# Kernel optimization log

Measured on AMD Instinct MI355X. Metric: run time of the kernel, lower is better.

The kernel has to match this reference:

```python
import jax, jax.numpy as jnp
import numpy as np

N, E, D, L, RBF = 20000, 320000, 128, 3, 64
CUTOFF = 5.0
LN_EPS = 1e-5


def setup_inputs() -> dict:
    key = jax.random.key(0)
    ks = jax.random.split(key, 20)
    s = 0.05
    inp = {
        'z': jax.random.normal(ks[0], (N, 64), jnp.float32),
        'pos': jax.random.normal(ks[1], (N, 3), jnp.float32),
        'edge_index': jax.random.randint(ks[2], (2, E), 0, N),
        'in_w': jax.random.normal(ks[3], (64, D), jnp.float32) * s,
        'in_b': jnp.zeros((D,), jnp.float32),
        'filt_w': jax.random.normal(ks[4], (RBF, 3 * D), jnp.float32) * s,
        'filt_b': jnp.zeros((3 * D,), jnp.float32),
        'inter_w1': jax.random.normal(ks[5], (L, D, D), jnp.float32) * s,
        'inter_b1': jnp.zeros((L, D), jnp.float32),
        'inter_w2': jax.random.normal(ks[6], (L, D, 3 * D), jnp.float32) * s,
        'inter_b2': jnp.zeros((L, 3 * D), jnp.float32),
        'mix_mu_w': jax.random.normal(ks[7], (L, D, 2 * D), jnp.float32) * s,
        'mix_w1': jax.random.normal(ks[8], (L, 2 * D, D), jnp.float32) * s,
        'mix_b1': jnp.zeros((L, D), jnp.float32),
        'mix_w2': jax.random.normal(ks[9], (L, D, 3 * D), jnp.float32) * s,
        'mix_b2': jnp.zeros((L, 3 * D), jnp.float32),
        'mu_proj_w': jnp.zeros((D,), jnp.float32),  # nn.init.constant_(0.0) in source
        'ln_g': jnp.ones((D,), jnp.float32),
        'ln_b': jnp.zeros((D,), jnp.float32),
    }
    return inp


def painn_forward(z, pos, in_w, in_b, filt_w, filt_b, inter_w1, inter_b1,
                  inter_w2, inter_b2, mix_mu_w, mix_w1, mix_b1, mix_w2, mix_b2,
                  mu_proj_w, ln_g, ln_b, edge_index):
    idx_i, idx_j = edge_index[0], edge_index[1]
    # edge geometry
    r_ij = pos[idx_j] - pos[idx_i]                               # [E,3]
    d_ij = jnp.maximum(jnp.linalg.norm(r_ij, axis=1, keepdims=True), 1e-8)  # [E,1]
    dir_ij = r_ij / d_ij                                          # [E,3]
    # gaussian smearing
    offset = jnp.linspace(0.0, CUTOFF, RBF).astype(jnp.float32)
    coeff = -0.5 / (offset[1] - offset[0]) ** 2
    phi = jnp.exp(coeff * (d_ij - offset) ** 2)                   # [E,RBF]
    # cosine cutoff
    xc = jnp.clip(d_ij / CUTOFF, 0.0, 1.0)
    fcut = 0.5 * (jnp.cos(jnp.pi * xc) + 1.0) * (xc < 1.0)        # [E,1]
    filters = (phi @ filt_w + filt_b) * fcut                      # [E,3D]
    filters = jnp.clip(jnp.nan_to_num(filters), -5.0, 5.0)
    Wij = filters[:, None, :]                                     # [E,1,3D]

    q = jax.nn.silu(z @ in_w + in_b)[:, None, :]                  # [N,1,D]
    mu = jnp.zeros((N, 3, D), q.dtype)                            # [N,3,D]

    for l in range(L):
        # interaction (edge gather -> gate -> scatter-add)
        x = jax.nn.silu(q @ inter_w1[l] + inter_b1[l]) @ inter_w2[l] + inter_b2[l]  # [N,1,3D]
        xj = x[idx_j] * Wij                                       # [E,1,3D]
        dq, dmuR, dmumu = jnp.split(xj, 3, axis=-1)               # each [E,1,D]
        muj = mu[idx_j]                                           # [E,3,D]
        q = q + jax.ops.segment_sum(dq, idx_i, num_segments=N)
        dmu = dmuR * dir_ij[:, :, None] + dmumu * muj             # [E,3,D]
        mu = mu + jax.ops.segment_sum(dmu, idx_i, num_segments=N)
        # intra-atomic mixing
        mu_mix = mu @ mix_mu_w[l]                                  # [N,3,2D]
        mu_V, mu_W = jnp.split(mu_mix, 2, axis=-1)                 # [N,3,D]
        mu_Vn = jnp.sqrt(jnp.sum(mu_V ** 2, axis=-2, keepdims=True) + 1e-8)  # [N,1,D]
        ctx = jnp.concatenate([q, mu_Vn], axis=-1)                 # [N,1,2D]
        xm = jax.nn.silu(ctx @ mix_w1[l] + mix_b1[l]) @ mix_w2[l] + mix_b2[l]  # [N,1,3D]
        dq_i, dmu_i, dqmu_i = jnp.split(xm, 3, axis=-1)
        q = q + dq_i + dqmu_i * jnp.sum(mu_V * mu_W, axis=1, keepdims=True)
        mu = mu + dmu_i * mu_W

    node_attr = jnp.clip(jnp.nan_to_num(q[:, 0, :]), -5.0, 5.0)   # [N,D]
    mean = jnp.mean(node_attr, axis=-1, keepdims=True)
    var = jnp.var(node_attr, axis=-1, keepdims=True)
    node_attr = (node_attr - mean) * jax.lax.rsqrt(var + LN_EPS) * ln_g + ln_b
    node_attr = jnp.nan_to_num(jnp.tanh(node_attr))

    mu = jnp.nan_to_num(mu)
    mu_node = jax.ops.segment_sum(mu[idx_j], idx_i, num_segments=N)  # [N,3,D]
    mu_node = jnp.clip(jnp.nan_to_num(mu_node), -5.0, 5.0)
    pos_attr = jnp.clip(jnp.nan_to_num(mu_node @ mu_proj_w), -5.0, 5.0)  # [N,3]
    return node_attr, pos_attr


def reference(z, pos, edge_index, in_w, in_b, filt_w, filt_b, inter_w1, inter_b1,
              inter_w2, inter_b2, mix_mu_w, mix_w1, mix_b1, mix_w2, mix_b2,
              mu_proj_w, ln_g, ln_b):
    return painn_forward(z, pos, in_w, in_b, filt_w, filt_b, inter_w1, inter_b1,
                         inter_w2, inter_b2, mix_mu_w, mix_w1, mix_b1, mix_w2,
                         mix_b2, mu_proj_w, ln_g, ln_b, edge_index)
```

## Files before the change

### kernel.cpp

```cpp
#include <hip/hip_runtime.h>
#include <math.h>

#ifndef M_PI
#define M_PI 3.14159265358979323846
#endif

static constexpr int N_NODES = 20000;
static constexpr int N_EDGES = 320000;
static constexpr int NLAYER  = 3;
static constexpr int NB_SCAN = (N_NODES + 255) / 256;
static constexpr int TAB_T   = 1024;

typedef _Float16 f16;
typedef __attribute__((ext_vector_type(2))) _Float16 f16x2;
typedef __attribute__((ext_vector_type(8))) _Float16 f16x8;
typedef __attribute__((ext_vector_type(4))) float f32x4;

__device__ __forceinline__ void storev(float* p, float v) { *p = v; }
__device__ __forceinline__ void storev(f16* p, float v)   { *p = (f16)v; }

__global__ void k_hist(const int* __restrict__ idx_i, int* __restrict__ cnt) {
  int e = blockIdx.x * 256 + threadIdx.x;
  if (e < N_EDGES) atomicAdd(&cnt[idx_i[e]], 1);
}

__global__ void k_scan_blk(const int* __restrict__ cnt, int* __restrict__ incl,
                           int* __restrict__ bsum) {
  __shared__ int buf[256];
  int t = threadIdx.x;
  int i = blockIdx.x * 256 + t;
  int v = (i < N_NODES) ? cnt[i] : 0;
  buf[t] = v;
  __syncthreads();
  #pragma unroll
  for (int off = 1; off < 256; off <<= 1) {
    int x = (t >= off) ? buf[t - off] : 0;
    __syncthreads();
    buf[t] += x;
    __syncthreads();
  }
  if (i < N_NODES) incl[i] = buf[t];
  if (t == 255) bsum[blockIdx.x] = buf[255];
}

__global__ void k_scan_top(int* __restrict__ bsum) {
  __shared__ int buf[128];
  int t = threadIdx.x;
  int v = (t < NB_SCAN) ? bsum[t] : 0;
  buf[t] = v;
  __syncthreads();
  #pragma unroll
  for (int off = 1; off < 128; off <<= 1) {
    int x = (t >= off) ? buf[t - off] : 0;
    __syncthreads();
    buf[t] += x;
    __syncthreads();
  }
  if (t <= NB_SCAN) bsum[t] = buf[t] - v;
}

__global__ void k_scan_add(const int* __restrict__ cnt, const int* __restrict__ incl,
                           const int* __restrict__ bsum, int* __restrict__ rs,
                           int* __restrict__ cur) {
  int i = blockIdx.x * 256 + threadIdx.x;
  if (i < N_NODES) {
    int v = bsum[blockIdx.x] + incl[i] - cnt[i];
    rs[i] = v;
    cur[i] = v;
  }
  if (i == 0) rs[N_NODES] = bsum[NB_SCAN];
}

__global__ void k_fill(const int* __restrict__ idx_i, int* __restrict__ cur, int* __restrict__ eidx) {
  int e = blockIdx.x * 256 + threadIdx.x;
  if (e < N_EDGES) {
    int p = atomicAdd(&cur[idx_i[e]], 1);
    eidx[p] = e;
  }
}

__global__ void k_edge_geom(const float* __restrict__ pos, const int* __restrict__ idx_all,
                            const int* __restrict__ eidx, float4* __restrict__ geo,
                            int* __restrict__ jperm) {
  int p = blockIdx.x * 256 + threadIdx.x;
  if (p >= N_EDGES) return;
  int e = eidx[p];
  int i = idx_all[e];
  int j = idx_all[N_EDGES + e];
  float rx = pos[j*3+0] - pos[i*3+0];
  float ry = pos[j*3+1] - pos[i*3+1];
  float rz = pos[j*3+2] - pos[i*3+2];
  float d = sqrtf(rx*rx + ry*ry + rz*rz);
  d = fmaxf(d, 1e-8f);
  float inv = 1.0f / d;
  geo[p] = make_float4(d, rx*inv, ry*inv, rz*inv);
  jperm[p] = j;
}

struct WJob { const float* src; f16* dst; int kshift; int ld; int col0; int nk; };
struct WJobs { WJob j[17]; };

__global__ void k_wt_all(WJobs jb) {
  WJob w = jb.j[blockIdx.y];
  int t = blockIdx.x * 256 + threadIdx.x;
  if (t >= w.nk) return;
  int K = 1 << w.kshift;
  int n = t >> w.kshift;
  int k = t & (K - 1);
  w.dst[t] = (f16)w.src[(size_t)k * w.ld + w.col0 + n];
}

__global__ __launch_bounds__(128) void k_tab(const f16* __restrict__ wt_f ,
                                             const float* __restrict__ bias,
                                             f16* __restrict__ tab) {
  __shared__ float ph[64];
  const int t = blockIdx.x;
  const float dist = 5.0f * (float)t / (float)(TAB_T - 1);
  const int tid = threadIdx.x;
  const float delta = 5.0f / 63.0f;
  const float coeff = -0.5f / (delta * delta);
  if (tid < 64) {
    float u = dist - delta * (float)tid;
    ph[tid] = expf(coeff * u * u);
  }
  __syncthreads();
  float xc = dist * 0.2f;
  float fc = (xc < 1.0f) ? 0.5f * (cosf((float)M_PI * xc) + 1.0f) : 0.0f;
  #pragma unroll
  for (int s = 0; s < 3; ++s) {
    int n = tid + s * 128;
    const f16* wr = wt_f + (size_t)n * 64;
    float acc = 0.f;
    #pragma unroll
    for (int k = 0; k < 64; ++k) acc += ph[k] * (float)wr[k];
    float v = (acc + bias[n]) * fc;
    v = fminf(fmaxf(v, -5.0f), 5.0f);
    tab[(size_t)t * 384 + n] = (f16)v;
  }
}

template<int EPI, typename AT, typename CT>
__global__ __launch_bounds__(256) void k_mgemm(
    const AT* __restrict__ A, const f16* __restrict__ Wt,
    const float* __restrict__ bias, CT* __restrict__ C,
    int M, int K, int ldc) {
  __shared__ f16 As[128 * 32];
  __shared__ f16 Bs[128 * 32];
  const int bm = blockIdx.x * 128;
  const int bn = blockIdx.y * 128;
  const int tid = threadIdx.x;
  const int wave = tid >> 6, lane = tid & 63;
  const int wm = (wave & 1) * 64, wn = (wave >> 1) * 64;
  const int lr = lane & 15;
  const int lk = lane >> 4;
  const int srow = tid >> 1;
  const int sc0 = (tid & 1) * 2;
  const int sw = (srow >> 1) & 3;
  f32x4 acc[4][4] = {};
  for (int k0 = 0; k0 < K; k0 += 32) {
    {
      int gm = bm + srow;
      f16x8 c0, c1;
      if (gm < M) {
        if constexpr (sizeof(AT) == 2) {
          const f16* ap = (const f16*)A + (size_t)gm * K + k0 + sc0 * 8;
          c0 = *(const f16x8*)ap;
          c1 = *(const f16x8*)(ap + 8);
        } else {
          const float* ap = (const float*)A + (size_t)gm * K + k0 + sc0 * 8;
          float4 v0 = ((const float4*)ap)[0];
          float4 v1 = ((const float4*)ap)[1];
          float4 v2 = ((const float4*)ap)[2];
          float4 v3 = ((const float4*)ap)[3];
          c0[0]=(f16)v0.x; c0[1]=(f16)v0.y; c0[2]=(f16)v0.z; c0[3]=(f16)v0.w;
          c0[4]=(f16)v1.x; c0[5]=(f16)v1.y; c0[6]=(f16)v1.z; c0[7]=(f16)v1.w;
          c1[0]=(f16)v2.x; c1[1]=(f16)v2.y; c1[2]=(f16)v2.z; c1[3]=(f16)v2.w;
          c1[4]=(f16)v3.x; c1[5]=(f16)v3.y; c1[6]=(f16)v3.z; c1[7]=(f16)v3.w;
        }
      } else {
        #pragma unroll
        for (int u = 0; u < 8; ++u) { c0[u] = (f16)0.f; c1[u] = (f16)0.f; }
      }
      *(f16x8*)&As[srow * 32 + ((sc0 ^ sw) << 3)]       = c0;
      *(f16x8*)&As[srow * 32 + (((sc0 + 1) ^ sw) << 3)] = c1;
    }
    {
      const f16* bp = Wt + (size_t)(bn + srow) * K + k0 + sc0 * 8;
      f16x8 b0 = *(const f16x8*)bp;
      f16x8 b1 = *(const f16x8*)(bp + 8);
      *(f16x8*)&Bs[srow * 32 + ((sc0 ^ sw) << 3)]       = b0;
      *(f16x8*)&Bs[srow * 32 + (((sc0 + 1) ^ sw) << 3)] = b1;
    }
    __syncthreads();
    f16x8 af[4], bf[4];
    #pragma unroll
    for (int mt = 0; mt < 4; ++mt) {
      int r = wm + mt * 16 + lr;
      af[mt] = *(const f16x8*)&As[r * 32 + ((lk ^ ((r >> 1) & 3)) << 3)];
    }
    #pragma unroll
    for (int nt = 0; nt < 4; ++nt) {
      int r = wn + nt * 16 + lr;
      bf[nt] = *(const f16x8*)&Bs[r * 32 + ((lk ^ ((r >> 1) & 3)) << 3)];
    }
    #pragma unroll
    for (int mt = 0; mt < 4; ++mt)
      #pragma unroll
      for (int nt = 0; nt < 4; ++nt)
        acc[mt][nt] = __builtin_amdgcn_mfma_f32_16x16x32_f16(af[mt], bf[nt], acc[mt][nt], 0, 0, 0);
    __syncthreads();
  }
  #pragma unroll
  for (int mt = 0; mt < 4; ++mt) {
    int gm0 = bm + wm + mt * 16 + lk * 4;
    #pragma unroll
    for (int nt = 0; nt < 4; ++nt) {
      int gn = bn + wn + nt * 16 + lr;
      float bv = bias ? bias[gn] : 0.0f;
      #pragma unroll
      for (int rr = 0; rr < 4; ++rr) {
        int gm = gm0 + rr;
        if (gm >= M) continue;
        float v = acc[mt][nt][rr] + bv;
        if (EPI == 1) v = v / (1.0f + expf(-v));
        storev(&C[(size_t)gm * ldc + gn], v);
      }
    }
  }
}

__global__ __launch_bounds__(256) void k_fused_i(
    const float* __restrict__ q, const f16* __restrict__ W1, const float* __restrict__ b1,
    const f16* __restrict__ W2, const float* __restrict__ b2,
    f16* __restrict__ xout, int M) {
  __shared__ f16 As[64 * 32];
  __shared__ f16 Hs[64 * 132];
  const int tid = threadIdx.x;
  const int wave = tid >> 6, lane = tid & 63;
  const int wm = (wave & 1) * 32, wn = (wave >> 1) * 64;
  const int lr = lane & 15, lk = lane >> 4;
  const int srow = tid >> 2, c8 = tid & 3;
  const int sw = (srow >> 1) & 3;
  const int bm = blockIdx.x * 64;
  f32x4 acc[2][4] = {};
  for (int k0 = 0; k0 < 128; k0 += 32) {
    {
      int gm = bm + srow;
      f16x8 c0;
      if (gm < M) {
        const float* ap = q + (size_t)gm * 128 + k0 + c8 * 8;
        float4 v0 = ((const float4*)ap)[0];
        float4 v1 = ((const float4*)ap)[1];
        c0[0]=(f16)v0.x; c0[1]=(f16)v0.y; c0[2]=(f16)v0.z; c0[3]=(f16)v0.w;
        c0[4]=(f16)v1.x; c0[5]=(f16)v1.y; c0[6]=(f16)v1.z; c0[7]=(f16)v1.w;
      } else {
        #pragma unroll
        for (int u = 0; u < 8; ++u) c0[u] = (f16)0.f;
      }
      *(f16x8*)&As[srow * 32 + ((c8 ^ sw) << 3)] = c0;
    }
    __syncthreads();
    f16x8 af[2], bf[4];
    #pragma unroll
    for (int mt = 0; mt < 2; ++mt) {
      int r = wm + mt * 16 + lr;
      af[mt] = *(const f16x8*)&As[r * 32 + ((lk ^ ((r >> 1) & 3)) << 3)];
    }
    #pragma unroll
    for (int nt = 0; nt < 4; ++nt)
      bf[nt] = *(const f16x8*)&W1[(size_t)(wn + nt * 16 + lr) * 128 + k0 + lk * 8];
    #pragma unroll
    for (int mt = 0; mt < 2; ++mt)
      #pragma unroll
      for (int nt = 0; nt < 4; ++nt)
        acc[mt][nt] = __builtin_amdgcn_mfma_f32_16x16x32_f16(af[mt], bf[nt], acc[mt][nt], 0, 0, 0);
    __syncthreads();
  }
  #pragma unroll
  for (int mt = 0; mt < 2; ++mt)
    #pragma unroll
    for (int nt = 0; nt < 4; ++nt) {
      int col = wn + nt * 16 + lr;
      float bv = b1[col];
      #pragma unroll
      for (int rr = 0; rr < 4; ++rr) {
        int row = wm + mt * 16 + lk * 4 + rr;
        float v = acc[mt][nt][rr] + bv;
        v = v / (1.0f + expf(-v));
        Hs[row * 132 + col] = (f16)v;
      }
    }
  __syncthreads();
  #pragma unroll
  for (int cc = 0; cc < 3; ++cc) {
    f32x4 a2[2][4] = {};
    for (int k0 = 0; k0 < 128; k0 += 32) {
      f16x8 af2[2], bf2[4];
      #pragma unroll
      for (int mt = 0; mt < 2; ++mt)
        af2[mt] = *(const f16x8*)&Hs[(wm + mt * 16 + lr) * 132 + k0 + lk * 8];
      #pragma unroll
      for (int nt = 0; nt < 4; ++nt)
        bf2[nt] = *(const f16x8*)&W2[(size_t)(cc * 128 + wn + nt * 16 + lr) * 128 + k0 + lk * 8];
      #pragma unroll
      for (int mt = 0; mt < 2; ++mt)
        #pragma unroll
        for (int nt = 0; nt < 4; ++nt)
          a2[mt][nt] = __builtin_amdgcn_mfma_f32_16x16x32_f16(af2[mt], bf2[nt], a2[mt][nt], 0, 0, 0);
    }
    #pragma unroll
    for (int mt = 0; mt < 2; ++mt)
      #pragma unroll
      for (int nt = 0; nt < 4; ++nt) {
        int gn = cc * 128 + wn + nt * 16 + lr;
        float bv = b2[gn];
        #pragma unroll
        for (int rr = 0; rr < 4; ++rr) {
          int gm = bm + wm + mt * 16 + lk * 4 + rr;
          if (gm >= M) continue;
          xout[(size_t)gm * 384 + gn] = (f16)(a2[mt][nt][rr] + bv);
        }
      }
  }
}

__global__ __launch_bounds__(256) void k_fused_mx(
    float* __restrict__ q, f16* __restrict__ mu,
    const f16* __restrict__ Wmu,
    const f16* __restrict__ W1, const float* __restrict__ b1,
    const f16* __restrict__ W2, const float* __restrict__ b2) {
  __shared__ __align__(16) char pool[50688 + 24576];
  f16* MM  = (f16*)pool;
  f16* As4 = (f16*)(pool + 50688);
  f16* VN  = (f16*)(pool + 50688);
  f16* HS  = (f16*)(pool + 50688 + 8192);

  const int tid = threadIdx.x;
  const int wave = tid >> 6, lane = tid & 63;
  const int lr = lane & 15, lk = lane >> 4;
  const int n0 = blockIdx.x * 32;
  const int r0 = n0 * 3;

  #pragma unroll
  for (int rep = 0; rep < 6; ++rep) {
    int idx = rep * 256 + tid;
    int row = idx >> 4;
    int g   = idx & 15;
    int kb = g >> 2, c8 = g & 3;
    f16x8 v = *(const f16x8*)(mu + (size_t)(r0 + row) * 128 + g * 8);
    *(f16x8*)&As4[((kb * 96 + row) << 5) + (((c8 ^ ((row >> 1) & 3))) << 3)] = v;
  }
  __syncthreads();

  const int wmA = (wave & 1) * 48;
  const int wnA0 = (wave >> 1) * 64;
  #pragma unroll
  for (int half = 0; half < 2; ++half) {
    f32x4 accA[3][4] = {};
    #pragma unroll
    for (int kk = 0; kk < 4; ++kk) {
      f16x8 af[3], bf[4];
      #pragma unroll
      for (int mt = 0; mt < 3; ++mt) {
        int r = wmA + mt * 16 + lr;
        af[mt] = *(const f16x8*)&As4[((kk * 96 + r) << 5) + ((lk ^ ((r >> 1) & 3)) << 3)];
      }
      #pragma unroll
      for (int nt = 0; nt < 4; ++nt)
        bf[nt] = *(const f16x8*)&Wmu[(size_t)(half * 128 + wnA0 + nt * 16 + lr) * 128 + kk * 32 + lk * 8];
      #pragma unroll
      for (int mt = 0; mt < 3; ++mt)
        #pragma unroll
        for (int nt = 0; nt < 4; ++nt)
          accA[mt][nt] = __builtin_amdgcn_mfma_f32_16x16x32_f16(af[mt], bf[nt], accA[mt][nt], 0, 0, 0);
    }
    #pragma unroll
    for (int mt = 0; mt < 3; ++mt)
      #pragma unroll
      for (int nt = 0; nt < 4; ++nt) {
        int col = half * 128 + wnA0 + nt * 16 + lr;
        #pragma unroll
        for (int rr = 0; rr < 4; ++rr) {
          int row = wmA + mt * 16 + lk * 4 + rr;
          MM[row * 264 + col] = (f16)accA[mt][nt][rr];
        }
      }
  }
  __syncthreads();

  #pragma unroll
  for (int rep = 0; rep < 16; ++rep) {
    int idx = rep * 256 + tid;
    int nn = idx >> 7, c = idx & 127;
    float V0 = (float)MM[(nn * 3 + 0) * 264 + c];
    float V1 = (float)MM[(nn * 3 + 1) * 264 + c];
    float V2 = (float)MM[(nn * 3 + 2) * 264 + c];
    float vnv = sqrtf(V0 * V0 + V1 * V1 + V2 * V2 + 1e-8f);
    int kb = c >> 5, c8 = (c >> 3) & 3, ce = c & 7;
    VN[((kb * 32 + nn) << 5) + ((c8 ^ ((nn >> 1) & 3)) << 3) + ce] = (f16)vnv;
  }
  __syncthreads();

  const int wmB = (wave & 1) * 16, wnB = (wave >> 1) * 64;
  f32x4 accB[4] = {};
  #pragma unroll
  for (int kk = 0; kk < 8; ++kk) {
    f16x8 af;
    int row = wmB + lr;
    if (kk < 4) {
      const float* qp_ = q + (size_t)(n0 + row) * 128 + kk * 32 + lk * 8;
      float4 v0 = ((const float4*)qp_)[0];
      float4 v1 = ((const float4*)qp_)[1];
      af[0]=(f16)v0.x; af[1]=(f16)v0.y; af[2]=(f16)v0.z; af[3]=(f16)v0.w;
      af[4]=(f16)v1.x; af[5]=(f16)v1.y; af[6]=(f16)v1.z; af[7]=(f16)v1.w;
    } else {
      af = *(const f16x8*)&VN[(((kk - 4) * 32 + row) << 5) + ((lk ^ ((row >> 1) & 3)) << 3)];
    }
    f16x8 bf[4];
    #pragma unroll
    for (int nt = 0; nt < 4; ++nt)
      bf[nt] = *(const f16x8*)&W1[(size_t)(wnB + nt * 16 + lr) * 256 + kk * 32 + lk * 8];
    #pragma unroll
    for (int nt = 0; nt < 4; ++nt)
      accB[nt] = __builtin_amdgcn_mfma_f32_16x16x32_f16(af, bf[nt], accB[nt], 0, 0, 0);
  }
  #pragma unroll
  for (int nt = 0; nt < 4; ++nt) {
    int col = wnB + nt * 16 + lr;
    float bv = b1[col];
    #pragma unroll
    for (int rr = 0; rr < 4; ++rr) {
      int row = wmB + lk * 4 + rr;
      float v = accB[nt][rr] + bv;
      v = v / (1.0f + expf(-v));
      HS[row * 132 + col] = (f16)v;
    }
  }
  __syncthreads();

  f32x4 accC[3][4] = {};
  #pragma unroll
  for (int cc = 0; cc < 3; ++cc)
    #pragma unroll
    for (int kk = 0; kk < 4; ++kk) {
      f16x8 af = *(const f16x8*)&HS[(wmB + lr) * 132 + kk * 32 + lk * 8];
      f16x8 bf[4];
      #pragma unroll
      for (int nt = 0; nt < 4; ++nt)
        bf[nt] = *(const f16x8*)&W2[(size_t)(cc * 128 + wnB + nt * 16 + lr) * 128 + kk * 32 + lk * 8];
      #pragma unroll
      for (int nt = 0; nt < 4; ++nt)
        accC[cc][nt] = __builtin_amdgcn_mfma_f32_16x16x32_f16(af, bf[nt], accC[cc][nt], 0, 0, 0);
    }
  #pragma unroll
  for (int nt = 0; nt < 4; ++nt) {
    int col = wnB + nt * 16 + lr;
    float b_dq = b2[col], b_dmu = b2[128 + col], b_dqmu = b2[256 + col];
    #pragma unroll
    for (int rr = 0; rr < 4; ++rr) {
      int nn = wmB + lk * 4 + rr;
      int gm = n0 + nn;
      float dq   = accC[0][nt][rr] + b_dq;
      float dmu  = accC[1][nt][rr] + b_dmu;
      float dqmu = accC[2][nt][rr] + b_dqmu;
      float V0 = (float)MM[(nn * 3 + 0) * 264 + col], W0 = (float)MM[(nn * 3 + 0) * 264 + 128 + col];
      float V1 = (float)MM[(nn * 3 + 1) * 264 + col], W1v = (float)MM[(nn * 3 + 1) * 264 + 128 + col];
      float V2 = (float)MM[(nn * 3 + 2) * 264 + col], W2v = (float)MM[(nn * 3 + 2) * 264 + 128 + col];
      float svw = V0 * W0 + V1 * W1v + V2 * W2v;
      size_t qi = (size_t)gm * 128 + col;
      q[qi] += dq + dqmu * svw;
      f16* mr = mu + (size_t)gm * 384;
      mr[col]       = (f16)((float)mr[col]       + dmu * W0);
      mr[128 + col] = (f16)((float)mr[128 + col] + dmu * W1v);
      mr[256 + col] = (f16)((float)mr[256 + col] + dmu * W2v);
    }
  }
}

__global__ __launch_bounds__(256) void k_edge_msg(
    const int* __restrict__ rs, const int* __restrict__ jperm,
    const f16* __restrict__ x, const f16* __restrict__ tab,
    const float4* __restrict__ geo, const f16* __restrict__ mu_in,
    float* __restrict__ q, f16* __restrict__ mu_out) {
  const int wid  = threadIdx.x >> 6;
  const int lane = threadIdx.x & 63;
  const int i = blockIdx.x * 4 + wid;
  if (i >= N_NODES) return;
  const int d0 = lane * 2;
  const float scale = (float)(TAB_T - 1) / 5.0f;
  float aqx = 0.f, aqy = 0.f;
  float a0x = 0.f, a0y = 0.f, a1x = 0.f, a1y = 0.f, a2x = 0.f, a2y = 0.f;
  const int s = rs[i], e = rs[i + 1];

  auto body = [&](float dx, float dy, float dz,
                  f16x2 ta0, f16x2 ta1, f16x2 ta2, f16x2 tb0, f16x2 tb1, f16x2 tb2,
                  f16x2 xv0, f16x2 xv1, f16x2 xv2, f16x2 mv0, f16x2 mv1, f16x2 mv2,
                  float fr) {
    float fo = 1.0f - fr;
    float W0x = fo * (float)ta0[0] + fr * (float)tb0[0];
    float W0y = fo * (float)ta0[1] + fr * (float)tb0[1];
    float W1x = fo * (float)ta1[0] + fr * (float)tb1[0];
    float W1y = fo * (float)ta1[1] + fr * (float)tb1[1];
    float W2x = fo * (float)ta2[0] + fr * (float)tb2[0];
    float W2y = fo * (float)ta2[1] + fr * (float)tb2[1];
    float m1x = (float)xv1[0] * W1x, m1y = (float)xv1[1] * W1y;
    float m2x = (float)xv2[0] * W2x, m2y = (float)xv2[1] * W2y;
    aqx = fmaf((float)xv0[0], W0x, aqx);
    aqy = fmaf((float)xv0[1], W0y, aqy);
    a0x += m1x * dx + m2x * (float)mv0[0];
    a0y += m1y * dx + m2y * (float)mv0[1];
    a1x += m1x * dy + m2x * (float)mv1[0];
    a1y += m1y * dy + m2y * (float)mv1[1];
    a2x += m1x * dz + m2x * (float)mv2[0];
    a2y += m1y * dz + m2y * (float)mv2[1];
  };

  int p = s;
  for (; p + 2 <= e; p += 2) {
    int jA = jperm[p], jB = jperm[p + 1];
    float4 gA = geo[p], gB = geo[p + 1];
    float uA = fminf(gA.x, 5.0f) * scale;
    float uB = fminf(gB.x, 5.0f) * scale;
    int tA = min((int)uA, TAB_T - 2);
    int tB = min((int)uB, TAB_T - 2);
    float frA = uA - (float)tA, frB = uB - (float)tB;
    const f16* taA = tab + (size_t)tA * 384;
    const f16* taB = tab + (size_t)tB * 384;
    const f16* xjA = x + (size_t)jA * 384;
    const f16* xjB = x + (size_t)jB * 384;
    const f16* mjA = mu_in + (size_t)jA * 384;
    const f16* mjB = mu_in + (size_t)jB * 384;
    f16x2 tA0 = *(const f16x2*)(taA + d0);
    f16x2 tA1 = *(const f16x2*)(taA + 128 + d0);
    f16x2 tA2 = *(const f16x2*)(taA + 256 + d0);
    f16x2 tA3 = *(const f16x2*)(taA + 384 + d0);
    f16x2 tA4 = *(const f16x2*)(taA + 512 + d0);
    f16x2 tA5 = *(const f16x2*)(taA + 640 + d0);
    f16x2 xA0 = *(const f16x2*)(xjA + d0);
    f16x2 xA1 = *(const f16x2*)(xjA + 128 + d0);
    f16x2 xA2 = *(const f16x2*)(xjA + 256 + d0);
    f16x2 mA0 = *(const f16x2*)(mjA + d0);
    f16x2 mA1 = *(const f16x2*)(mjA + 128 + d0);
    f16x2 mA2 = *(const f16x2*)(mjA + 256 + d0);
    f16x2 tB0 = *(const f16x2*)(taB + d0);
    f16x2 tB1 = *(const f16x2*)(taB + 128 + d0);
    f16x2 tB2 = *(const f16x2*)(taB + 256 + d0);
    f16x2 tB3 = *(const f16x2*)(taB + 384 + d0);
    f16x2 tB4 = *(const f16x2*)(taB + 512 + d0);
    f16x2 tB5 = *(const f16x2*)(taB + 640 + d0);
    f16x2 xB0 = *(const f16x2*)(xjB + d0);
    f16x2 xB1 = *(const f16x2*)(xjB + 128 + d0);
    f16x2 xB2 = *(const f16x2*)(xjB + 256 + d0);
    f16x2 mB0 = *(const f16x2*)(mjB + d0);
    f16x2 mB1 = *(const f16x2*)(mjB + 128 + d0);
    f16x2 mB2 = *(const f16x2*)(mjB + 256 + d0);
    body(gA.y, gA.z, gA.w, tA0, tA1, tA2, tA3, tA4, tA5,
         xA0, xA1, xA2, mA0, mA1, mA2, frA);
    body(gB.y, gB.z, gB.w, tB0, tB1, tB2, tB3, tB4, tB5,
         xB0, xB1, xB2, mB0, mB1, mB2, frB);
  }
  for (; p < e; ++p) {
    int j = jperm[p];
    float4 g = geo[p];
    float u = fminf(g.x, 5.0f) * scale;
    int t0 = min((int)u, TAB_T - 2);
    float fr = u - (float)t0;
    const f16* ta = tab + (size_t)t0 * 384;
    const f16* xj = x + (size_t)j * 384;
    const f16* mj = mu_in + (size_t)j * 384;
    body(g.y, g.z, g.w,
         *(const f16x2*)(ta + d0), *(const f16x2*)(ta + 128 + d0), *(const f16x2*)(ta + 256 + d0),
         *(const f16x2*)(ta + 384 + d0), *(const f16x2*)(ta + 512 + d0), *(const f16x2*)(ta + 640 + d0),
         *(const f16x2*)(xj + d0), *(const f16x2*)(xj + 128 + d0), *(const f16x2*)(xj + 256 + d0),
         *(const f16x2*)(mj + d0), *(const f16x2*)(mj + 128 + d0), *(const f16x2*)(mj + 256 + d0),
         fr);
  }

  float* qp = q + (size_t)i * 128 + d0;
  float2 qv = *(float2*)qp;
  qv.x += aqx; qv.y += aqy;
  *(float2*)qp = qv;
  const f16* min_ = mu_in + (size_t)i * 384;
  f16* mout = mu_out + (size_t)i * 384;
  f16x2 o0, o1, o2;
  f16x2 i0 = *(const f16x2*)(min_ + d0);
  f16x2 i1 = *(const f16x2*)(min_ + 128 + d0);
  f16x2 i2 = *(const f16x2*)(min_ + 256 + d0);
  o0[0] = (f16)((float)i0[0] + a0x); o0[1] = (f16)((float)i0[1] + a0y);
  o1[0] = (f16)((float)i1[0] + a1x); o1[1] = (f16)((float)i1[1] + a1y);
  o2[0] = (f16)((float)i2[0] + a2x); o2[1] = (f16)((float)i2[1] + a2y);
  *(f16x2*)(mout + d0)       = o0;
  *(f16x2*)(mout + 128 + d0) = o1;
  *(f16x2*)(mout + 256 + d0) = o2;
}

__global__ __launch_bounds__(256) void k_posattr(
    const int* __restrict__ rs, const int* __restrict__ jperm,
    const f16* __restrict__ mu, const float* __restrict__ w, float* __restrict__ pos_out) {
  const int wid  = threadIdx.x >> 6;
  const int lane = threadIdx.x & 63;
  const int i = blockIdx.x * 4 + wid;
  if (i >= N_NODES) return;
  const int d0 = lane * 2;
  float a0x = 0.f, a0y = 0.f, a1x = 0.f, a1y = 0.f, a2x = 0.f, a2y = 0.f;
  const int s = rs[i], e = rs[i + 1];
  int p = s;
  for (; p + 2 <= e; p += 2) {
    int jA = jperm[p], jB = jperm[p + 1];
    const f16* mA = mu + (size_t)jA * 384;
    const f16* mB = mu + (size_t)jB * 384;
    f16x2 A0 = *(const f16x2*)(mA + d0);
    f16x2 A1 = *(const f16x2*)(mA + 128 + d0);
    f16x2 A2 = *(const f16x2*)(mA + 256 + d0);
    f16x2 B0 = *(const f16x2*)(mB + d0);
    f16x2 B1 = *(const f16x2*)(mB + 128 + d0);
    f16x2 B2 = *(const f16x2*)(mB + 256 + d0);
    a0x += (float)A0[0] + (float)B0[0]; a0y += (float)A0[1] + (float)B0[1];
    a1x += (float)A1[0] + (float)B1[0]; a1y += (float)A1[1] + (float)B1[1];
    a2x += (float)A2[0] + (float)B2[0]; a2y += (float)A2[1] + (float)B2[1];
  }
  for (; p < e; ++p) {
    int j = jperm[p];
    const f16* mj = mu + (size_t)j * 384;
    f16x2 A0 = *(const f16x2*)(mj + d0);
    f16x2 A1 = *(const f16x2*)(mj + 128 + d0);
    f16x2 A2 = *(const f16x2*)(mj + 256 + d0);
    a0x += (float)A0[0]; a0y += (float)A0[1];
    a1x += (float)A1[0]; a1y += (float)A1[1];
    a2x += (float)A2[0]; a2y += (float)A2[1];
  }
  float wx = w[d0], wy = w[d0 + 1];
  float s0 = fminf(fmaxf(a0x, -5.f), 5.f) * wx + fminf(fmaxf(a0y, -5.f), 5.f) * wy;
  float s1 = fminf(fmaxf(a1x, -5.f), 5.f) * wx + fminf(fmaxf(a1y, -5.f), 5.f) * wy;
  float s2 = fminf(fmaxf(a2x, -5.f), 5.f) * wx + fminf(fmaxf(a2y, -5.f), 5.f) * wy;
  #pragma unroll
  for (int off = 32; off > 0; off >>= 1) {
    s0 += __shfl_down(s0, off, 64);
    s1 += __shfl_down(s1, off, 64);
    s2 += __shfl_down(s2, off, 64);
  }
  if (lane == 0) {
    pos_out[(size_t)i * 3 + 0] = fminf(fmaxf(s0, -5.f), 5.f);
    pos_out[(size_t)i * 3 + 1] = fminf(fmaxf(s1, -5.f), 5.f);
    pos_out[(size_t)i * 3 + 2] = fminf(fmaxf(s2, -5.f), 5.f);
  }
}

__global__ __launch_bounds__(256) void k_ln(const float* __restrict__ q, const float* __restrict__ g,
                                            const float* __restrict__ b, float* __restrict__ out) {
  const int wid = threadIdx.x >> 6, lane = threadIdx.x & 63;
  const int n = blockIdx.x * 4 + wid;
  if (n >= N_NODES) return;
  const int d0 = lane * 2;
  float2 v = *(const float2*)(q + (size_t)n * 128 + d0);
  float v0 = fminf(fmaxf(v.x, -5.f), 5.f);
  float v1 = fminf(fmaxf(v.y, -5.f), 5.f);
  float s = v0 + v1, s2 = v0 * v0 + v1 * v1;
  #pragma unroll
  for (int off = 32; off > 0; off >>= 1) {
    s  += __shfl_down(s,  off, 64);
    s2 += __shfl_down(s2, off, 64);
  }
  s  = __shfl(s,  0, 64);
  s2 = __shfl(s2, 0, 64);
  float mean = s * (1.0f / 128.0f);
  float var  = s2 * (1.0f / 128.0f) - mean * mean;
  float r = rsqrtf(var + 1e-5f);
  out[(size_t)n * 128 + d0]     = tanhf((v0 - mean) * r * g[d0]     + b[d0]);
  out[(size_t)n * 128 + d0 + 1] = tanhf((v1 - mean) * r * g[d0 + 1] + b[d0 + 1]);
}

extern "C" void kernel_launch(void* const* d_in, const int* in_sizes, int n_in,
                              void* d_out, int out_size, void* d_ws, size_t ws_size,
                              hipStream_t stream) {
  const float* z         = (const float*)d_in[0];
  const float* pos       = (const float*)d_in[1];
  const int*   edge_idx  = (const int*)d_in[2];
  const float* in_w      = (const float*)d_in[3];
  const float* in_b      = (const float*)d_in[4];
  const float* filt_w    = (const float*)d_in[5];
  const float* filt_b    = (const float*)d_in[6];
  const float* inter_w1  = (const float*)d_in[7];
  const float* inter_b1  = (const float*)d_in[8];
  const float* inter_w2  = (const float*)d_in[9];
  const float* inter_b2  = (const float*)d_in[10];
  const float* mix_mu_w  = (const float*)d_in[11];
  const float* mix_w1    = (const float*)d_in[12];
  const float* mix_b1    = (const float*)d_in[13];
  const float* mix_w2    = (const float*)d_in[14];
  const float* mix_b2    = (const float*)d_in[15];
  const float* mu_proj_w = (const float*)d_in[16];
  const float* ln_g      = (const float*)d_in[17];
  const float* ln_b      = (const float*)d_in[18];

  char* base = (char*)d_ws;
  size_t off = 0;
  auto alloc = [&](size_t bytes) -> char* {
    char* p = base + off;
    off += (bytes + 255) & ~(size_t)255;
    return p;
  };
  float*  q     = (float*)alloc((size_t)N_NODES * 128 * 4);
  f16*    x16   = (f16*)alloc((size_t)N_NODES * 384 * 2);
  f16*    mu_a  = (f16*)alloc((size_t)N_NODES * 384 * 2);
  f16*    mu_b  = (f16*)alloc((size_t)N_NODES * 384 * 2);
  float4* geo   = (float4*)alloc((size_t)N_EDGES * 16);
  int*    cnt   = (int*)alloc((size_t)N_NODES * 4);
  int*    incl  = (int*)alloc((size_t)N_NODES * 4);
  int*    bsum  = (int*)alloc(128 * 4);
  int*    rs    = (int*)alloc((size_t)(N_NODES + 1) * 4);
  int*    cur   = (int*)alloc((size_t)N_NODES * 4);
  int*    eidx  = (int*)alloc((size_t)N_EDGES * 4);
  int*    jperm = (int*)alloc((size_t)N_EDGES * 4);
  f16*    tab   = (f16*)alloc((size_t)TAB_T * 384 * 2);
  f16* wt_in = (f16*)alloc((size_t)128 * 64 * 2);
  f16* wt_f  = (f16*)alloc((size_t)384 * 64 * 2);
  f16* wt_i1 = (f16*)alloc((size_t)3 * 128 * 128 * 2);
  f16* wt_i2 = (f16*)alloc((size_t)3 * 384 * 128 * 2);
  f16* wt_mu = (f16*)alloc((size_t)3 * 256 * 128 * 2);
  f16* wt_x1 = (f16*)alloc((size_t)3 * 128 * 256 * 2);
  f16* wt_x2 = (f16*)alloc((size_t)3 * 384 * 128 * 2);
  if (off > ws_size) return;

  float* out_node = (float*)d_out;
  float* out_pos  = (float*)d_out + (size_t)N_NODES * 128;

  {
    WJobs jb;
    int ji = 0;
    jb.j[ji++] = {in_w,   wt_in, 6, 128, 0, 128 * 64};
    jb.j[ji++] = {filt_w, wt_f,  6, 384, 0, 384 * 64};
    for (int l = 0; l < 3; ++l)
      jb.j[ji++] = {inter_w1 + (size_t)l*128*128, wt_i1 + (size_t)l*128*128, 7, 128, 0, 128*128};
    for (int l = 0; l < 3; ++l)
      jb.j[ji++] = {inter_w2 + (size_t)l*128*384, wt_i2 + (size_t)l*384*128, 7, 384, 0, 384*128};
    for (int l = 0; l < 3; ++l)
      jb.j[ji++] = {mix_mu_w + (size_t)l*128*256, wt_mu + (size_t)l*256*128, 7, 256, 0, 256*128};
    for (int l = 0; l < 3; ++l)
      jb.j[ji++] = {mix_w1 + (size_t)l*256*128, wt_x1 + (size_t)l*128*256, 8, 128, 0, 128*256};
    for (int l = 0; l < 3; ++l)
      jb.j[ji++] = {mix_w2 + (size_t)l*128*384, wt_x2 + (size_t)l*384*128, 7, 384, 0, 384*128};
    dim3 g(192, 17);
    k_wt_all<<<g, 256, 0, stream>>>(jb);
  }

  k_tab<<<TAB_T, 128, 0, stream>>>(wt_f, filt_b, tab);

  hipMemsetAsync(cnt, 0, (size_t)N_NODES * 4, stream);
  k_hist<<<N_EDGES / 256, 256, 0, stream>>>(edge_idx, cnt);
  k_scan_blk<<<NB_SCAN, 256, 0, stream>>>(cnt, incl, bsum);
  k_scan_top<<<1, 128, 0, stream>>>(bsum);
  k_scan_add<<<NB_SCAN, 256, 0, stream>>>(cnt, incl, bsum, rs, cur);
  k_fill<<<N_EDGES / 256, 256, 0, stream>>>(edge_idx, cur, eidx);

  k_edge_geom<<<N_EDGES / 256, 256, 0, stream>>>(pos, edge_idx, eidx, geo, jperm);

  dim3 ge((N_NODES + 127) / 128, 1);
  k_mgemm<1, float, float><<<ge, 256, 0, stream>>>(z, wt_in, in_b, q, N_NODES, 64, 128);
  hipMemsetAsync(mu_a, 0, (size_t)N_NODES * 384 * 2, stream);

  f16* mu_cur = mu_a;
  f16* mu_nxt = mu_b;
  const int gn4 = (N_NODES + 3) / 4;
  const int gf  = (N_NODES + 63) / 64;
  const int gmx = N_NODES / 32;
  for (int l = 0; l < NLAYER; ++l) {
    k_fused_i<<<gf, 256, 0, stream>>>(q, wt_i1 + (size_t)l*128*128, inter_b1 + (size_t)l*128,
                                      wt_i2 + (size_t)l*384*128, inter_b2 + (size_t)l*384,
                                      x16, N_NODES);
    k_edge_msg<<<gn4, 256, 0, stream>>>(rs, jperm, x16, tab, geo, mu_cur, q, mu_nxt);
    { f16* t = mu_cur; mu_cur = mu_nxt; mu_nxt = t; }
    k_fused_mx<<<gmx, 256, 0, stream>>>(q, mu_cur, wt_mu + (size_t)l*256*128,
                                        wt_x1 + (size_t)l*128*256, mix_b1 + (size_t)l*128,
                                        wt_x2 + (size_t)l*384*128, mix_b2 + (size_t)l*384);
  }

  k_posattr<<<gn4, 256, 0, stream>>>(rs, jperm, mu_cur, mu_proj_w, out_pos);
  k_ln<<<gn4, 256, 0, stream>>>(q, ln_g, ln_b, out_node);
}
```

Measured before the change: 613.5 us.

## Merge setup kernels, skip zero mu work in first layer, fuse output kernels

```diff
diff --git a/kernel.cpp b/kernel.cpp
--- a/kernel.cpp
+++ b/kernel.cpp
@@ -71,22 +71,14 @@
   if (i == 0) rs[N_NODES] = bsum[NB_SCAN];
 }
 
-__global__ void k_fill(const int* __restrict__ idx_i, int* __restrict__ cur, int* __restrict__ eidx) {
+__global__ void k_fill_geom(const int* __restrict__ idx_all, const float* __restrict__ pos,
+                            int* __restrict__ cur, float4* __restrict__ geo,
+                            int* __restrict__ jperm) {
   int e = blockIdx.x * 256 + threadIdx.x;
-  if (e < N_EDGES) {
-    int p = atomicAdd(&cur[idx_i[e]], 1);
-    eidx[p] = e;
-  }
-}
-
-__global__ void k_edge_geom(const float* __restrict__ pos, const int* __restrict__ idx_all,
-                            const int* __restrict__ eidx, float4* __restrict__ geo,
-                            int* __restrict__ jperm) {
-  int p = blockIdx.x * 256 + threadIdx.x;
-  if (p >= N_EDGES) return;
-  int e = eidx[p];
+  if (e >= N_EDGES) return;
   int i = idx_all[e];
   int j = idx_all[N_EDGES + e];
+  int p = atomicAdd(&cur[i], 1);
   float rx = pos[j*3+0] - pos[i*3+0];
   float ry = pos[j*3+1] - pos[i*3+1];
   float rz = pos[j*3+2] - pos[i*3+2];
@@ -98,25 +90,26 @@
 }
 
 struct WJob { const float* src; f16* dst; int kshift; int ld; int col0; int nk; };
-struct WJobs { WJob j[17]; };
-
-__global__ void k_wt_all(WJobs jb) {
-  WJob w = jb.j[blockIdx.y];
-  int t = blockIdx.x * 256 + threadIdx.x;
-  if (t >= w.nk) return;
-  int K = 1 << w.kshift;
-  int n = t >> w.kshift;
-  int k = t & (K - 1);
-  w.dst[t] = (f16)w.src[(size_t)k * w.ld + w.col0 + n];
-}
-
-__global__ __launch_bounds__(128) void k_tab(const f16* __restrict__ wt_f ,
-                                             const float* __restrict__ bias,
-                                             f16* __restrict__ tab) {
+struct WJobs { WJob j[16]; };
+
+__global__ __launch_bounds__(256) void k_prep(WJobs jb, const float* __restrict__ filt_w,
+                                              const float* __restrict__ filt_b,
+                                              f16* __restrict__ tab) {
+  if (blockIdx.y < 16) {
+    WJob w = jb.j[blockIdx.y];
+    int t = blockIdx.x * 256 + threadIdx.x;
+    if (t >= w.nk) return;
+    int K = 1 << w.kshift;
+    int n = t >> w.kshift;
+    int k = t & (K - 1);
+    w.dst[t] = (f16)w.src[(size_t)k * w.ld + w.col0 + n];
+    return;
+  }
+  if (blockIdx.x >= 128) return;
+  const int t = (blockIdx.y - 16) * 128 + blockIdx.x;
   __shared__ float ph[64];
-  const int t = blockIdx.x;
+  const int tid = threadIdx.x;
   const float dist = 5.0f * (float)t / (float)(TAB_T - 1);
-  const int tid = threadIdx.x;
   const float delta = 5.0f / 63.0f;
   const float coeff = -0.5f / (delta * delta);
   if (tid < 64) {
@@ -126,14 +119,11 @@
   __syncthreads();
   float xc = dist * 0.2f;
   float fc = (xc < 1.0f) ? 0.5f * (cosf((float)M_PI * xc) + 1.0f) : 0.0f;
-  #pragma unroll
-  for (int s = 0; s < 3; ++s) {
-    int n = tid + s * 128;
-    const f16* wr = wt_f + (size_t)n * 64;
+  for (int n = tid; n < 384; n += 256) {
     float acc = 0.f;
     #pragma unroll
-    for (int k = 0; k < 64; ++k) acc += ph[k] * (float)wr[k];
-    float v = (acc + bias[n]) * fc;
+    for (int k = 0; k < 64; ++k) acc += ph[k] * filt_w[k * 384 + n];
+    float v = (acc + filt_b[n]) * fc;
     v = fminf(fmaxf(v, -5.0f), 5.0f);
     tab[(size_t)t * 384 + n] = (f16)v;
   }
@@ -477,6 +467,7 @@
   }
 }
 
+template<bool HASMU>
 __global__ __launch_bounds__(256) void k_edge_msg(
     const int* __restrict__ rs, const int* __restrict__ jperm,
     const f16* __restrict__ x, const f16* __restrict__ tab,
@@ -492,116 +483,104 @@
   float a0x = 0.f, a0y = 0.f, a1x = 0.f, a1y = 0.f, a2x = 0.f, a2y = 0.f;
   const int s = rs[i], e = rs[i + 1];
 
-  auto body = [&](float dx, float dy, float dz,
-                  f16x2 ta0, f16x2 ta1, f16x2 ta2, f16x2 tb0, f16x2 tb1, f16x2 tb2,
-                  f16x2 xv0, f16x2 xv1, f16x2 xv2, f16x2 mv0, f16x2 mv1, f16x2 mv2,
-                  float fr) {
-    float fo = 1.0f - fr;
+  for (int p = s; p < e; ++p) {
+    int j = jperm[p];
+    float4 g = geo[p];
+    float u = fminf(g.x, 5.0f) * scale;
+    int t0 = min((int)u, TAB_T - 2);
+    float fr = u - (float)t0, fo = 1.0f - fr;
+    const f16* ta = tab + (size_t)t0 * 384;
+    const f16* xj = x + (size_t)j * 384;
+    f16x2 ta0 = *(const f16x2*)(ta + d0);
+    f16x2 ta1 = *(const f16x2*)(ta + 128 + d0);
+    f16x2 tb0 = *(const f16x2*)(ta + 384 + d0);
+    f16x2 tb1 = *(const f16x2*)(ta + 512 + d0);
+    f16x2 xv0 = *(const f16x2*)(xj + d0);
+    f16x2 xv1 = *(const f16x2*)(xj + 128 + d0);
     float W0x = fo * (float)ta0[0] + fr * (float)tb0[0];
     float W0y = fo * (float)ta0[1] + fr * (float)tb0[1];
     float W1x = fo * (float)ta1[0] + fr * (float)tb1[0];
     float W1y = fo * (float)ta1[1] + fr * (float)tb1[1];
-    float W2x = fo * (float)ta2[0] + fr * (float)tb2[0];
-    float W2y = fo * (float)ta2[1] + fr * (float)tb2[1];
     float m1x = (float)xv1[0] * W1x, m1y = (float)xv1[1] * W1y;
-    float m2x = (float)xv2[0] * W2x, m2y = (float)xv2[1] * W2y;
     aqx = fmaf((float)xv0[0], W0x, aqx);
     aqy = fmaf((float)xv0[1], W0y, aqy);
-    a0x += m1x * dx + m2x * (float)mv0[0];
-    a0y += m1y * dx + m2y * (float)mv0[1];
-    a1x += m1x * dy + m2x * (float)mv1[0];
-    a1y += m1y * dy + m2y * (float)mv1[1];
-    a2x += m1x * dz + m2x * (float)mv2[0];
-    a2y += m1y * dz + m2y * (float)mv2[1];
-  };
-
-  int p = s;
-  for (; p + 2 <= e; p += 2) {
-    int jA = jperm[p], jB = jperm[p + 1];
-    float4 gA = geo[p], gB = geo[p + 1];
-    float uA = fminf(gA.x, 5.0f) * scale;
-    float uB = fminf(gB.x, 5.0f) * scale;
-    int tA = min((int)uA, TAB_T - 2);
-    int tB = min((int)uB, TAB_T - 2);
-    float frA = uA - (float)tA, frB = uB - (float)tB;
-    const f16* taA = tab + (size_t)tA * 384;
-    const f16* taB = tab + (size_t)tB * 384;
-    const f16* xjA = x + (size_t)jA * 384;
-    const f16* xjB = x + (size_t)jB * 384;
-    const f16* mjA = mu_in + (size_t)jA * 384;
-    const f16* mjB = mu_in + (size_t)jB * 384;
-    f16x2 tA0 = *(const f16x2*)(taA + d0);
-    f16x2 tA1 = *(const f16x2*)(taA + 128 + d0);
-    f16x2 tA2 = *(const f16x2*)(taA + 256 + d0);
-    f16x2 tA3 = *(const f16x2*)(taA + 384 + d0);
-    f16x2 tA4 = *(const f16x2*)(taA + 512 + d0);
-    f16x2 tA5 = *(const f16x2*)(taA + 640 + d0);
-    f16x2 xA0 = *(const f16x2*)(xjA + d0);
-    f16x2 xA1 = *(const f16x2*)(xjA + 128 + d0);
-    f16x2 xA2 = *(const f16x2*)(xjA + 256 + d0);
-    f16x2 mA0 = *(const f16x2*)(mjA + d0);
-    f16x2 mA1 = *(const f16x2*)(mjA + 128 + d0);
-    f16x2 mA2 = *(const f16x2*)(mjA + 256 + d0);
-    f16x2 tB0 = *(const f16x2*)(taB + d0);
-    f16x2 tB1 = *(const f16x2*)(taB + 128 + d0);
-    f16x2 tB2 = *(const f16x2*)(taB + 256 + d0);
-    f16x2 tB3 = *(const f16x2*)(taB + 384 + d0);
-    f16x2 tB4 = *(const f16x2*)(taB + 512 + d0);
-    f16x2 tB5 = *(const f16x2*)(taB + 640 + d0);
-    f16x2 xB0 = *(const f16x2*)(xjB + d0);
-    f16x2 xB1 = *(const f16x2*)(xjB + 128 + d0);
-    f16x2 xB2 = *(const f16x2*)(xjB + 256 + d0);
-    f16x2 mB0 = *(const f16x2*)(mjB + d0);
-    f16x2 mB1 = *(const f16x2*)(mjB + 128 + d0);
-    f16x2 mB2 = *(const f16x2*)(mjB + 256 + d0);
-    body(gA.y, gA.z, gA.w, tA0, tA1, tA2, tA3, tA4, tA5,
-         xA0, xA1, xA2, mA0, mA1, mA2, frA);
-    body(gB.y, gB.z, gB.w, tB0, tB1, tB2, tB3, tB4, tB5,
-         xB0, xB1, xB2, mB0, mB1, mB2, frB);
-  }
-  for (; p < e; ++p) {
-    int j = jperm[p];
-    float4 g = geo[p];
-    float u = fminf(g.x, 5.0f) * scale;
-    int t0 = min((int)u, TAB_T - 2);
-    float fr = u - (float)t0;
-    const f16* ta = tab + (size_t)t0 * 384;
-    const f16* xj = x + (size_t)j * 384;
-    const f16* mj = mu_in + (size_t)j * 384;
-    body(g.y, g.z, g.w,
-         *(const f16x2*)(ta + d0), *(const f16x2*)(ta + 128 + d0), *(const f16x2*)(ta + 256 + d0),
-         *(const f16x2*)(ta + 384 + d0), *(const f16x2*)(ta + 512 + d0), *(const f16x2*)(ta + 640 + d0),
-         *(const f16x2*)(xj + d0), *(const f16x2*)(xj + 128 + d0), *(const f16x2*)(xj + 256 + d0),
-         *(const f16x2*)(mj + d0), *(const f16x2*)(mj + 128 + d0), *(const f16x2*)(mj + 256 + d0),
-         fr);
+    if constexpr (HASMU) {
+      f16x2 ta2 = *(const f16x2*)(ta + 256 + d0);
+      f16x2 tb2 = *(const f16x2*)(ta + 640 + d0);
+      f16x2 xv2 = *(const f16x2*)(xj + 256 + d0);
+      const f16* mj = mu_in + (size_t)j * 384;
+      f16x2 mv0 = *(const f16x2*)(mj + d0);
+      f16x2 mv1 = *(const f16x2*)(mj + 128 + d0);
+      f16x2 mv2 = *(const f16x2*)(mj + 256 + d0);
+      float W2x = fo * (float)ta2[0] + fr * (float)tb2[0];
+      float W2y = fo * (float)ta2[1] + fr * (float)tb2[1];
+      float m2x = (float)xv2[0] * W2x, m2y = (float)xv2[1] * W2y;
+      a0x += m1x * g.y + m2x * (float)mv0[0];
+      a0y += m1y * g.y + m2y * (float)mv0[1];
+      a1x += m1x * g.z + m2x * (float)mv1[0];
+      a1y += m1y * g.z + m2y * (float)mv1[1];
+      a2x += m1x * g.w + m2x * (float)mv2[0];
+      a2y += m1y * g.w + m2y * (float)mv2[1];
+    } else {
+      a0x += m1x * g.y; a0y += m1y * g.y;
+      a1x += m1x * g.z; a1y += m1y * g.z;
+      a2x += m1x * g.w; a2y += m1y * g.w;
+    }
   }
 
   float* qp = q + (size_t)i * 128 + d0;
   float2 qv = *(float2*)qp;
   qv.x += aqx; qv.y += aqy;
   *(float2*)qp = qv;
-  const f16* min_ = mu_in + (size_t)i * 384;
   f16* mout = mu_out + (size_t)i * 384;
   f16x2 o0, o1, o2;
-  f16x2 i0 = *(const f16x2*)(min_ + d0);
-  f16x2 i1 = *(const f16x2*)(min_ + 128 + d0);
-  f16x2 i2 = *(const f16x2*)(min_ + 256 + d0);
-  o0[0] = (f16)((float)i0[0] + a0x); o0[1] = (f16)((float)i0[1] + a0y);
-  o1[0] = (f16)((float)i1[0] + a1x); o1[1] = (f16)((float)i1[1] + a1y);
-  o2[0] = (f16)((float)i2[0] + a2x); o2[1] = (f16)((float)i2[1] + a2y);
+  if constexpr (HASMU) {
+    const f16* min_ = mu_in + (size_t)i * 384;
+    f16x2 i0 = *(const f16x2*)(min_ + d0);
+    f16x2 i1 = *(const f16x2*)(min_ + 128 + d0);
+    f16x2 i2 = *(const f16x2*)(min_ + 256 + d0);
+    o0[0] = (f16)((float)i0[0] + a0x); o0[1] = (f16)((float)i0[1] + a0y);
+    o1[0] = (f16)((float)i1[0] + a1x); o1[1] = (f16)((float)i1[1] + a1y);
+    o2[0] = (f16)((float)i2[0] + a2x); o2[1] = (f16)((float)i2[1] + a2y);
+  } else {
+    o0[0] = (f16)a0x; o0[1] = (f16)a0y;
+    o1[0] = (f16)a1x; o1[1] = (f16)a1y;
+    o2[0] = (f16)a2x; o2[1] = (f16)a2y;
+  }
   *(f16x2*)(mout + d0)       = o0;
   *(f16x2*)(mout + 128 + d0) = o1;
   *(f16x2*)(mout + 256 + d0) = o2;
 }
 
-__global__ __launch_bounds__(256) void k_posattr(
+__global__ __launch_bounds__(256) void k_outputs(
     const int* __restrict__ rs, const int* __restrict__ jperm,
-    const f16* __restrict__ mu, const float* __restrict__ w, float* __restrict__ pos_out) {
+    const f16* __restrict__ mu, const float* __restrict__ w, float* __restrict__ pos_out,
+    const float* __restrict__ q, const float* __restrict__ g_, const float* __restrict__ b_,
+    float* __restrict__ out_node) {
   const int wid  = threadIdx.x >> 6;
   const int lane = threadIdx.x & 63;
   const int i = blockIdx.x * 4 + wid;
   if (i >= N_NODES) return;
   const int d0 = lane * 2;
+  if (blockIdx.y == 1) {
+    float2 v = *(const float2*)(q + (size_t)i * 128 + d0);
+    float v0 = fminf(fmaxf(v.x, -5.f), 5.f);
+    float v1 = fminf(fmaxf(v.y, -5.f), 5.f);
+    float s = v0 + v1, s2 = v0 * v0 + v1 * v1;
+    #pragma unroll
+    for (int off = 32; off > 0; off >>= 1) {
+      s  += __shfl_down(s,  off, 64);
+      s2 += __shfl_down(s2, off, 64);
+    }
+    s  = __shfl(s,  0, 64);
+    s2 = __shfl(s2, 0, 64);
+    float mean = s * (1.0f / 128.0f);
+    float var  = s2 * (1.0f / 128.0f) - mean * mean;
+    float r = rsqrtf(var + 1e-5f);
+    out_node[(size_t)i * 128 + d0]     = tanhf((v0 - mean) * r * g_[d0]     + b_[d0]);
+    out_node[(size_t)i * 128 + d0 + 1] = tanhf((v1 - mean) * r * g_[d0 + 1] + b_[d0 + 1]);
+    return;
+  }
   float a0x = 0.f, a0y = 0.f, a1x = 0.f, a1y = 0.f, a2x = 0.f, a2y = 0.f;
   const int s = rs[i], e = rs[i + 1];
   int p = s;
@@ -644,30 +623,6 @@
     pos_out[(size_t)i * 3 + 1] = fminf(fmaxf(s1, -5.f), 5.f);
     pos_out[(size_t)i * 3 + 2] = fminf(fmaxf(s2, -5.f), 5.f);
   }
-}
-
-__global__ __launch_bounds__(256) void k_ln(const float* __restrict__ q, const float* __restrict__ g,
-                                            const float* __restrict__ b, float* __restrict__ out) {
-  const int wid = threadIdx.x >> 6, lane = threadIdx.x & 63;
-  const int n = blockIdx.x * 4 + wid;
-  if (n >= N_NODES) return;
-  const int d0 = lane * 2;
-  float2 v = *(const float2*)(q + (size_t)n * 128 + d0);
-  float v0 = fminf(fmaxf(v.x, -5.f), 5.f);
-  float v1 = fminf(fmaxf(v.y, -5.f), 5.f);
-  float s = v0 + v1, s2 = v0 * v0 + v1 * v1;
-  #pragma unroll
-  for (int off = 32; off > 0; off >>= 1) {
-    s  += __shfl_down(s,  off, 64);
-    s2 += __shfl_down(s2, off, 64);
-  }
-  s  = __shfl(s,  0, 64);
-  s2 = __shfl(s2, 0, 64);
-  float mean = s * (1.0f / 128.0f);
-  float var  = s2 * (1.0f / 128.0f) - mean * mean;
-  float r = rsqrtf(var + 1e-5f);
-  out[(size_t)n * 128 + d0]     = tanhf((v0 - mean) * r * g[d0]     + b[d0]);
-  out[(size_t)n * 128 + d0 + 1] = tanhf((v1 - mean) * r * g[d0 + 1] + b[d0 + 1]);
 }
 
 extern "C" void kernel_launch(void* const* d_in, const int* in_sizes, int n_in,
@@ -710,11 +665,9 @@
   int*    bsum  = (int*)alloc(128 * 4);
   int*    rs    = (int*)alloc((size_t)(N_NODES + 1) * 4);
   int*    cur   = (int*)alloc((size_t)N_NODES * 4);
-  int*    eidx  = (int*)alloc((size_t)N_EDGES * 4);
   int*    jperm = (int*)alloc((size_t)N_EDGES * 4);
   f16*    tab   = (f16*)alloc((size_t)TAB_T * 384 * 2);
   f16* wt_in = (f16*)alloc((size_t)128 * 64 * 2);
-  f16* wt_f  = (f16*)alloc((size_t)384 * 64 * 2);
   f16* wt_i1 = (f16*)alloc((size_t)3 * 128 * 128 * 2);
   f16* wt_i2 = (f16*)alloc((size_t)3 * 384 * 128 * 2);
   f16* wt_mu = (f16*)alloc((size_t)3 * 256 * 128 * 2);
@@ -728,8 +681,7 @@
   {
     WJobs jb;
     int ji = 0;
-    jb.j[ji++] = {in_w,   wt_in, 6, 128, 0, 128 * 64};
-    jb.j[ji++] = {filt_w, wt_f,  6, 384, 0, 384 * 64};
+    jb.j[ji++] = {in_w, wt_in, 6, 128, 0, 128 * 64};
     for (int l = 0; l < 3; ++l)
       jb.j[ji++] = {inter_w1 + (size_t)l*128*128, wt_i1 + (size_t)l*128*128, 7, 128, 0, 128*128};
     for (int l = 0; l < 3; ++l)
@@ -740,24 +692,19 @@
       jb.j[ji++] = {mix_w1 + (size_t)l*256*128, wt_x1 + (size_t)l*128*256, 8, 128, 0, 128*256};
     for (int l = 0; l < 3; ++l)
       jb.j[ji++] = {mix_w2 + (size_t)l*128*384, wt_x2 + (size_t)l*384*128, 7, 384, 0, 384*128};
-    dim3 g(192, 17);
-    k_wt_all<<<g, 256, 0, stream>>>(jb);
-  }
-
-  k_tab<<<TAB_T, 128, 0, stream>>>(wt_f, filt_b, tab);
+    dim3 g(192, 24);
+    k_prep<<<g, 256, 0, stream>>>(jb, filt_w, filt_b, tab);
+  }
 
   hipMemsetAsync(cnt, 0, (size_t)N_NODES * 4, stream);
   k_hist<<<N_EDGES / 256, 256, 0, stream>>>(edge_idx, cnt);
   k_scan_blk<<<NB_SCAN, 256, 0, stream>>>(cnt, incl, bsum);
   k_scan_top<<<1, 128, 0, stream>>>(bsum);
   k_scan_add<<<NB_SCAN, 256, 0, stream>>>(cnt, incl, bsum, rs, cur);
-  k_fill<<<N_EDGES / 256, 256, 0, stream>>>(edge_idx, cur, eidx);
-
-  k_edge_geom<<<N_EDGES / 256, 256, 0, stream>>>(pos, edge_idx, eidx, geo, jperm);
+  k_fill_geom<<<N_EDGES / 256, 256, 0, stream>>>(edge_idx, pos, cur, geo, jperm);
 
   dim3 ge((N_NODES + 127) / 128, 1);
   k_mgemm<1, float, float><<<ge, 256, 0, stream>>>(z, wt_in, in_b, q, N_NODES, 64, 128);
-  hipMemsetAsync(mu_a, 0, (size_t)N_NODES * 384 * 2, stream);
 
   f16* mu_cur = mu_a;
   f16* mu_nxt = mu_b;
@@ -768,13 +715,17 @@
     k_fused_i<<<gf, 256, 0, stream>>>(q, wt_i1 + (size_t)l*128*128, inter_b1 + (size_t)l*128,
                                       wt_i2 + (size_t)l*384*128, inter_b2 + (size_t)l*384,
                                       x16, N_NODES);
-    k_edge_msg<<<gn4, 256, 0, stream>>>(rs, jperm, x16, tab, geo, mu_cur, q, mu_nxt);
+    if (l == 0)
+      k_edge_msg<false><<<gn4, 256, 0, stream>>>(rs, jperm, x16, tab, geo, mu_cur, q, mu_nxt);
+    else
+      k_edge_msg<true><<<gn4, 256, 0, stream>>>(rs, jperm, x16, tab, geo, mu_cur, q, mu_nxt);
     { f16* t = mu_cur; mu_cur = mu_nxt; mu_nxt = t; }
     k_fused_mx<<<gmx, 256, 0, stream>>>(q, mu_cur, wt_mu + (size_t)l*256*128,
                                         wt_x1 + (size_t)l*128*256, mix_b1 + (size_t)l*128,
                                         wt_x2 + (size_t)l*384*128, mix_b2 + (size_t)l*384);
   }
 
-  k_posattr<<<gn4, 256, 0, stream>>>(rs, jperm, mu_cur, mu_proj_w, out_pos);
-  k_ln<<<gn4, 256, 0, stream>>>(q, ln_g, ln_b, out_node);
-}
+  dim3 go(gn4, 2);
+  k_outputs<<<go, 256, 0, stream>>>(rs, jperm, mu_cur, mu_proj_w, out_pos,
+                                    q, ln_g, ln_b, out_node);
+}
```

New measurement: 587.3 us. -4.3%, faster.
